# Kernel tuning notes

Hardware: AMD Instinct MI355X
Metric: run time of the kernel (lower is better)

The kernel has to match this reference:

```python
import jax, jax.numpy as jnp
import numpy as np

N_WIRES = 6
N_LAYERS = 4
P = 2
IN_C = 3
OUT_C = 16
B, H, W = 8, 224, 224


def rot_matrix(phi, theta, omega):
    # PennyLane Rot(phi, theta, omega) = RZ(omega) RY(theta) RZ(phi)
    c = jnp.cos(theta * 0.5)
    s = jnp.sin(theta * 0.5)
    ep = jnp.exp(-0.5j * (phi + omega))  # e^{-i(phi+omega)/2}
    em = jnp.exp(-0.5j * (phi - omega))  # e^{-i(phi-omega)/2}
    row0 = jnp.stack([ep * c, -jnp.conj(em) * s])
    row1 = jnp.stack([em * s, jnp.conj(ep) * c])
    return jnp.stack([row0, row1]).astype(jnp.complex64)  # [2,2]


def apply_1q(state, U, wire):
    # state: [N] + [2]*N_WIRES, U: [2,2]
    s = jnp.moveaxis(state, 1 + wire, -1)
    s = jnp.einsum('...i,ji->...j', s, U)
    return jnp.moveaxis(s, -1, 1 + wire)


def apply_cnot(state, c, t):
    s = jnp.moveaxis(state, (1 + c, 1 + t), (-2, -1))
    s = jnp.stack([s[..., 0, :], s[..., 1, ::-1]], axis=-2)
    return jnp.moveaxis(s, (-2, -1), (1 + c, 1 + t))


def _forward(x, weights, fc_w, fc_b, ln_g, ln_b):
    Bx, C, Hx, Wx = x.shape
    p = P
    Hp, Wp = Hx // p, Wx // p
    # unfold + mean over each p x p patch == average pooling
    xm = x.reshape(Bx, C, Hp, p, Wp, p).mean(axis=(3, 5))        # [B,C,Hp,Wp]
    xm = xm.transpose(0, 2, 3, 1).reshape(-1, C)                  # [N,C]
    angles = jnp.pad(xm, ((0, 0), (0, N_WIRES - C)))              # C < n_wires branch
    # AngleEmbedding (RX): product state, RX(a)|0> = [cos(a/2), -i sin(a/2)]
    half = angles * 0.5
    kets = jnp.stack([jnp.cos(half).astype(jnp.complex64),
                      (-1j) * jnp.sin(half).astype(jnp.complex64)], axis=-1)  # [N,6,2]
    state = kets[:, 0]
    for w in range(1, N_WIRES):
        state = jnp.einsum('n...,nj->n...j', state, kets[:, w])  # [N]+[2]*w
    # StronglyEntanglingLayers: Rot on each wire, then CNOT ring with range r
    for l in range(N_LAYERS):
        for w in range(N_WIRES):
            U = rot_matrix(weights[l, w, 0], weights[l, w, 1], weights[l, w, 2])
            state = apply_1q(state, U, w)
        r = (l % (N_WIRES - 1)) + 1
        for w in range(N_WIRES):
            state = apply_cnot(state, w, (w + r) % N_WIRES)
    # <Z_i> expectation values
    probs = state.real ** 2 + state.imag ** 2                     # [N]+[2]*6
    exps = []
    for w in range(N_WIRES):
        axes = tuple(a for a in range(1, N_WIRES + 1) if a != 1 + w)
        pw = probs.sum(axis=axes)                                 # [N,2]
        exps.append(pw[:, 0] - pw[:, 1])
    q = jnp.stack(exps, axis=-1)                                  # [N,6]
    y = q @ fc_w.T + fc_b                                         # [N,16]
    mu = y.mean(-1, keepdims=True)
    var = ((y - mu) ** 2).mean(-1, keepdims=True)
    y = (y - mu) / jnp.sqrt(var + 1e-5) * ln_g + ln_b
    y = jax.nn.relu(y)
    y = y.reshape(Bx, Hp, Wp, OUT_C).transpose(0, 3, 1, 2)        # [B,16,Hp,Wp]
    # F.interpolate(scale=p, bilinear, align_corners=False) == half-pixel bilinear
    return jax.image.resize(y, (Bx, OUT_C, Hx, Wx), method='bilinear')


def setup_inputs() -> dict:
    key = jax.random.key(0)
    ks = jax.random.split(key, 4)
    x = jax.random.normal(ks[0], (B, IN_C, H, W), jnp.float32)
    weights = jax.random.uniform(ks[1], (N_LAYERS, N_WIRES, 3), jnp.float32,
                                 0.0, 2.0 * np.pi)
    fc_w = jax.random.normal(ks[2], (OUT_C, N_WIRES), jnp.float32) * 0.4
    fc_b = jax.random.normal(ks[3], (OUT_C,), jnp.float32) * 0.1
    ln_g = jnp.ones((OUT_C,), jnp.float32)
    ln_b = jnp.zeros((OUT_C,), jnp.float32)
    return {'x': x, 'weights': weights, 'fc_w': fc_w, 'fc_b': fc_b,
            'ln_g': ln_g, 'ln_b': ln_b}


def reference(x, weights, fc_w, fc_b, ln_g, ln_b):
    return _forward(x, weights, fc_w, fc_b, ln_g, ln_b)
```

## Files before the change

### kernel.cpp

```cpp
#include <hip/hip_runtime.h>
#include <math.h>


#define HP 112
#define WP 112

__global__ __launch_bounds__(512) void build_G(const float* __restrict__ wts,
                                               float* __restrict__ S) {
    __shared__ float  U[24][8];
    __shared__ float2 cs[64][9];
    int t = threadIdx.x;
    int lane = t & 63, wv = t >> 6;

    if (t < 24) {
        float phi = wts[t*3+0], th = wts[t*3+1], om = wts[t*3+2];
        float cth, sth, cap, sap, cam, sam;
        sincosf(0.5f*th, &sth, &cth);
        sincosf(0.5f*(phi+om), &sap, &cap);
        sincosf(0.5f*(phi-om), &sam, &cam);
        U[t][0] =  cap*cth; U[t][1] = -sap*cth;
        U[t][2] = -cam*sth; U[t][3] = -sam*sth;
        U[t][4] =  cam*sth; U[t][5] = -sam*sth;
        U[t][6] =  cap*cth; U[t][7] =  sap*cth;
    }
    __syncthreads();

    float2 v = make_float2((lane == (wv << 3)) ? 1.0f : 0.0f, 0.0f);

    for (int l = 0; l < 4; ++l) {
        for (int w = 0; w < 6; ++w) {
            int g = l*6 + w, m = 1 << (5 - w);
            bool hi = (lane & m) != 0;
            float csr = hi ? U[g][6] : U[g][0], csi = hi ? U[g][7] : U[g][1];
            float cpr = hi ? U[g][4] : U[g][2], cpi = hi ? U[g][5] : U[g][3];
            float px = __shfl_xor(v.x, m), py = __shfl_xor(v.y, m);
            v = make_float2(csr*v.x - csi*v.y + cpr*px - cpi*py,
                            csr*v.y + csi*v.x + cpr*py + cpi*px);
        }
        int r = l % 5 + 1;
        for (int w = 0; w < 6; ++w) {
            int mc = 1 << (5 - w), mt = 1 << (5 - ((w + r) % 6));
            float px = __shfl_xor(v.x, mt), py = __shfl_xor(v.y, mt);
            if (lane & mc) v = make_float2(px, py);
        }
    }

    cs[lane][wv] = v;
    __syncthreads();

    if (t < 384) {
        int w = t >> 6, a = (t >> 3) & 7, bb = t & 7;
        if (a <= bb) {
            int mw = 1 << (5 - w);
            float re = 0.f, im = 0.f;
            for (int s = 0; s < 64; ++s) {
                float z = (s & mw) ? -1.f : 1.f;
                float2 va = cs[s][a], vb = cs[s][bb];
                re += z * (va.x*vb.x + va.y*vb.y);
                im += z * (va.x*vb.y - va.y*vb.x);
            }
            int d = (__popc(a) - __popc(bb)) & 3;
            float g = (d == 0) ? re : (d == 1) ? -im : (d == 2) ? -re : im;
            int idx = 8*a - (a*(a-1))/2 + (bb - a);
            S[w*36 + idx] = (a == bb) ? g : 2.0f*g;
        }
    }
}

__global__ __launch_bounds__(256) void fused(
    const float* __restrict__ x, const float* __restrict__ fcw,
    const float* __restrict__ fcb, const float* __restrict__ lng,
    const float* __restrict__ lnb, const float* __restrict__ S,
    float* __restrict__ out) {

    __shared__ __align__(16) float Ss[216];
    __shared__ float fcwS[96], fcbS[16], lngS[16], lnbS[16];
    __shared__ float yS[16][10][18];

    int tid = threadIdx.x;
    int b   = blockIdx.z;
    int ow0 = blockIdx.x * 32, oh0 = blockIdx.y * 16;
    int w0  = blockIdx.x * 16, k0  = blockIdx.y * 8;

    if (tid < 216) Ss[tid] = S[tid];
    for (int i = tid; i < 96;  i += 256) fcwS[i] = fcw[i];
    if (tid < 16) { fcbS[tid] = fcb[tid]; lngS[tid] = lng[tid]; lnbS[tid] = lnb[tid]; }
    __syncthreads();

    if (tid < 180) {
        int pr = tid / 18, pc = tid % 18;
        int ih = min(max(k0 - 1 + pr, 0), HP - 1);
        int iw = min(max(w0 - 1 + pc, 0), WP - 1);

        float m[3];
        #pragma unroll
        for (int c = 0; c < 3; ++c) {
            const float2* px = reinterpret_cast<const float2*>(
                x + (((b*3 + c)*224 + 2*ih)*224 + 2*iw));
            float2 r0 = px[0], r1 = px[112];
            m[c] = 0.25f * (r0.x + r0.y + r1.x + r1.y);
        }

        float cc[3], ssn[3];
        #pragma unroll
        for (int c = 0; c < 3; ++c) __sincosf(0.5f*m[c], &ssn[c], &cc[c]);

        float r8[8] = { cc[0]*cc[1]*cc[2], cc[0]*cc[1]*ssn[2],
                        cc[0]*ssn[1]*cc[2], cc[0]*ssn[1]*ssn[2],
                        ssn[0]*cc[1]*cc[2], ssn[0]*cc[1]*ssn[2],
                        ssn[0]*ssn[1]*cc[2], ssn[0]*ssn[1]*ssn[2] };

        float p[36];
        {
            int k = 0;
            #pragma unroll
            for (int a = 0; a < 8; ++a)
                #pragma unroll
                for (int bb = a; bb < 8; ++bb) p[k++] = r8[a]*r8[bb];
        }

        float q[6];
        #pragma unroll
        for (int w = 0; w < 6; ++w) {
            const float4* S4 = reinterpret_cast<const float4*>(Ss + w*36);
            float acc = 0.f;
            #pragma unroll
            for (int j = 0; j < 9; ++j) {
                float4 s4 = S4[j];
                acc += s4.x*p[j*4+0] + s4.y*p[j*4+1]
                     + s4.z*p[j*4+2] + s4.w*p[j*4+3];
            }
            q[w] = acc;
        }

        float y[16]; float mu = 0.f;
        #pragma unroll
        for (int c = 0; c < 16; ++c) {
            float v = fcbS[c];
            #pragma unroll
            for (int w = 0; w < 6; ++w) v += fcwS[c*6 + w] * q[w];
            y[c] = v; mu += v;
        }
        mu *= 0.0625f;
        float var = 0.f;
        #pragma unroll
        for (int c = 0; c < 16; ++c) { float d = y[c] - mu; var += d*d; }
        var *= 0.0625f;
        float inv = 1.0f / sqrtf(var + 1e-5f);
        #pragma unroll
        for (int c = 0; c < 16; ++c) {
            float vv = (y[c] - mu) * inv * lngS[c] + lnbS[c];
            yS[c][pr][pc] = fmaxf(vv, 0.f);
        }
    }
    __syncthreads();

    #pragma unroll
    for (int k = 0; k < 8; ++k) {
        int it = tid + k * 256;
        int c = it >> 7, rem = it & 127, ohl = rem >> 3, owg = rem & 7;
        int oh = oh0 + ohl, ow = ow0 + owg * 4;
        int kh = oh >> 1, kw = ow >> 1;

        int ha, hb; float wha;
        if (oh & 1) { ha = kh;     hb = min(kh + 1, HP - 1); wha = 0.75f; }
        else        { ha = max(kh - 1, 0); hb = kh;          wha = 0.25f; }
        ha -= (k0 - 1); hb -= (k0 - 1);
        float whb = 1.f - wha;

        int t0 = max(kw - 1, 0)      - (w0 - 1);
        int t1 = kw                  - (w0 - 1);
        int t2 = kw + 1              - (w0 - 1);
        int t3 = min(kw + 2, WP - 1) - (w0 - 1);

        float va0 = wha * yS[c][ha][t0] + whb * yS[c][hb][t0];
        float va1 = wha * yS[c][ha][t1] + whb * yS[c][hb][t1];
        float va2 = wha * yS[c][ha][t2] + whb * yS[c][hb][t2];
        float va3 = wha * yS[c][ha][t3] + whb * yS[c][hb][t3];

        float4 o;
        o.x = 0.25f * va0 + 0.75f * va1;
        o.y = 0.75f * va1 + 0.25f * va2;
        o.z = 0.25f * va1 + 0.75f * va2;
        o.w = 0.75f * va2 + 0.25f * va3;
        *reinterpret_cast<float4*>(out + (((b*16 + c)*224 + oh)*224 + ow)) = o;
    }
}

extern "C" void kernel_launch(void* const* d_in, const int* in_sizes, int n_in,
                              void* d_out, int out_size, void* d_ws, size_t ws_size,
                              hipStream_t stream) {
    const float* x   = (const float*)d_in[0];
    const float* wts = (const float*)d_in[1];
    const float* fcw = (const float*)d_in[2];
    const float* fcb = (const float*)d_in[3];
    const float* lng = (const float*)d_in[4];
    const float* lnb = (const float*)d_in[5];
    float* S   = (float*)d_ws;
    float* out = (float*)d_out;

    build_G<<<1, 512, 0, stream>>>(wts, S);
    fused<<<dim3(7, 14, 8), 256, 0, stream>>>(x, fcw, fcb, lng, lnb, S, out);
}
```

Measured before the change: 84.46 us.

## Fold circuit matrix construction into every block of the fused kernel

Removes the separate single-block build_G launch and has each block of the fused kernel recompute the 6x36 observable matrix itself. Four wavefronts each simulate two basis states of the circuit, and the matrix goes straight into shared memory. The x loads are issued before that work so their latency overlaps it. This saves a kernel launch and the global round trip, but repeats the small circuit simulation in all 784 blocks and adds two barriers before the main work.

```diff
diff --git a/kernel.cpp b/kernel.cpp
--- a/kernel.cpp
+++ b/kernel.cpp
@@ -5,27 +5,59 @@
 #define HP 112
 #define WP 112
 
-__global__ __launch_bounds__(512) void build_G(const float* __restrict__ wts,
-                                               float* __restrict__ S) {
+static __device__ const unsigned char TRI_A[36] = {
+    0,0,0,0,0,0,0,0, 1,1,1,1,1,1,1, 2,2,2,2,2,2, 3,3,3,3,3, 4,4,4,4, 5,5,5, 6,6, 7};
+static __device__ const unsigned char TRI_B[36] = {
+    0,1,2,3,4,5,6,7, 1,2,3,4,5,6,7, 2,3,4,5,6,7, 3,4,5,6,7, 4,5,6,7, 5,6,7, 6,7, 7};
+
+__global__ __launch_bounds__(256) void fused(
+    const float* __restrict__ x, const float* __restrict__ wts,
+    const float* __restrict__ fcw, const float* __restrict__ fcb,
+    const float* __restrict__ lng, const float* __restrict__ lnb,
+    float* __restrict__ out) {
+
     __shared__ float  U[24][8];
     __shared__ float2 cs[64][9];
-    int t = threadIdx.x;
-    int lane = t & 63, wv = t >> 6;
-
-    if (t < 24) {
-        float phi = wts[t*3+0], th = wts[t*3+1], om = wts[t*3+2];
+    __shared__ __align__(16) float Ss[216];
+    __shared__ float fcwS[96], fcbS[16], lngS[16], lnbS[16];
+    __shared__ float yS[16][10][18];
+
+    int tid  = threadIdx.x;
+    int lane = tid & 63, wv = tid >> 6;
+    int b    = blockIdx.z;
+    int ow0  = blockIdx.x * 32, oh0 = blockIdx.y * 16;
+    int w0   = blockIdx.x * 16, k0  = blockIdx.y * 8;
+
+    float2 xr[3][2];
+    int pr = tid / 18, pc = tid % 18;
+    if (tid < 180) {
+        int ih = min(max(k0 - 1 + pr, 0), HP - 1);
+        int iw = min(max(w0 - 1 + pc, 0), WP - 1);
+        #pragma unroll
+        for (int c = 0; c < 3; ++c) {
+            const float2* px = reinterpret_cast<const float2*>(
+                x + (((b*3 + c)*224 + 2*ih)*224 + 2*iw));
+            xr[c][0] = px[0]; xr[c][1] = px[112];
+        }
+    }
+    for (int i = tid; i < 96; i += 256) fcwS[i] = fcw[i];
+    if (tid < 16) { fcbS[tid] = fcb[tid]; lngS[tid] = lng[tid]; lnbS[tid] = lnb[tid]; }
+
+    if (tid < 24) {
+        float phi = wts[tid*3+0], th = wts[tid*3+1], om = wts[tid*3+2];
         float cth, sth, cap, sap, cam, sam;
-        sincosf(0.5f*th, &sth, &cth);
-        sincosf(0.5f*(phi+om), &sap, &cap);
-        sincosf(0.5f*(phi-om), &sam, &cam);
-        U[t][0] =  cap*cth; U[t][1] = -sap*cth;
-        U[t][2] = -cam*sth; U[t][3] = -sam*sth;
-        U[t][4] =  cam*sth; U[t][5] = -sam*sth;
-        U[t][6] =  cap*cth; U[t][7] =  sap*cth;
-    }
-    __syncthreads();
-
-    float2 v = make_float2((lane == (wv << 3)) ? 1.0f : 0.0f, 0.0f);
+        __sincosf(0.5f*th, &sth, &cth);
+        __sincosf(0.5f*(phi+om), &sap, &cap);
+        __sincosf(0.5f*(phi-om), &sam, &cam);
+        U[tid][0] =  cap*cth; U[tid][1] = -sap*cth;
+        U[tid][2] = -cam*sth; U[tid][3] = -sam*sth;
+        U[tid][4] =  cam*sth; U[tid][5] = -sam*sth;
+        U[tid][6] =  cap*cth; U[tid][7] =  sap*cth;
+    }
+    __syncthreads();
+
+    float2 v0 = make_float2((lane == (wv << 3))       ? 1.0f : 0.0f, 0.0f);
+    float2 v1 = make_float2((lane == ((wv + 4) << 3)) ? 1.0f : 0.0f, 0.0f);
 
     for (int l = 0; l < 4; ++l) {
         for (int w = 0; w < 6; ++w) {
@@ -33,77 +65,50 @@
             bool hi = (lane & m) != 0;
             float csr = hi ? U[g][6] : U[g][0], csi = hi ? U[g][7] : U[g][1];
             float cpr = hi ? U[g][4] : U[g][2], cpi = hi ? U[g][5] : U[g][3];
-            float px = __shfl_xor(v.x, m), py = __shfl_xor(v.y, m);
-            v = make_float2(csr*v.x - csi*v.y + cpr*px - cpi*py,
-                            csr*v.y + csi*v.x + cpr*py + cpi*px);
+            float p0x = __shfl_xor(v0.x, m), p0y = __shfl_xor(v0.y, m);
+            float p1x = __shfl_xor(v1.x, m), p1y = __shfl_xor(v1.y, m);
+            v0 = make_float2(csr*v0.x - csi*v0.y + cpr*p0x - cpi*p0y,
+                             csr*v0.y + csi*v0.x + cpr*p0y + cpi*p0x);
+            v1 = make_float2(csr*v1.x - csi*v1.y + cpr*p1x - cpi*p1y,
+                             csr*v1.y + csi*v1.x + cpr*p1y + cpi*p1x);
         }
         int r = l % 5 + 1;
         for (int w = 0; w < 6; ++w) {
             int mc = 1 << (5 - w), mt = 1 << (5 - ((w + r) % 6));
-            float px = __shfl_xor(v.x, mt), py = __shfl_xor(v.y, mt);
-            if (lane & mc) v = make_float2(px, py);
-        }
-    }
-
-    cs[lane][wv] = v;
-    __syncthreads();
-
-    if (t < 384) {
-        int w = t >> 6, a = (t >> 3) & 7, bb = t & 7;
-        if (a <= bb) {
-            int mw = 1 << (5 - w);
-            float re = 0.f, im = 0.f;
-            for (int s = 0; s < 64; ++s) {
-                float z = (s & mw) ? -1.f : 1.f;
-                float2 va = cs[s][a], vb = cs[s][bb];
-                re += z * (va.x*vb.x + va.y*vb.y);
-                im += z * (va.x*vb.y - va.y*vb.x);
-            }
-            int d = (__popc(a) - __popc(bb)) & 3;
-            float g = (d == 0) ? re : (d == 1) ? -im : (d == 2) ? -re : im;
-            int idx = 8*a - (a*(a-1))/2 + (bb - a);
-            S[w*36 + idx] = (a == bb) ? g : 2.0f*g;
-        }
-    }
-}
-
-__global__ __launch_bounds__(256) void fused(
-    const float* __restrict__ x, const float* __restrict__ fcw,
-    const float* __restrict__ fcb, const float* __restrict__ lng,
-    const float* __restrict__ lnb, const float* __restrict__ S,
-    float* __restrict__ out) {
-
-    __shared__ __align__(16) float Ss[216];
-    __shared__ float fcwS[96], fcbS[16], lngS[16], lnbS[16];
-    __shared__ float yS[16][10][18];
-
-    int tid = threadIdx.x;
-    int b   = blockIdx.z;
-    int ow0 = blockIdx.x * 32, oh0 = blockIdx.y * 16;
-    int w0  = blockIdx.x * 16, k0  = blockIdx.y * 8;
-
-    if (tid < 216) Ss[tid] = S[tid];
-    for (int i = tid; i < 96;  i += 256) fcwS[i] = fcw[i];
-    if (tid < 16) { fcbS[tid] = fcb[tid]; lngS[tid] = lng[tid]; lnbS[tid] = lnb[tid]; }
+            float p0x = __shfl_xor(v0.x, mt), p0y = __shfl_xor(v0.y, mt);
+            float p1x = __shfl_xor(v1.x, mt), p1y = __shfl_xor(v1.y, mt);
+            if (lane & mc) { v0 = make_float2(p0x, p0y); v1 = make_float2(p1x, p1y); }
+        }
+    }
+    cs[lane][wv]     = v0;
+    cs[lane][wv + 4] = v1;
+    __syncthreads();
+
+    if (tid < 216) {
+        int w = tid / 36, idx = tid - 36*w;
+        int a = TRI_A[idx], bb = TRI_B[idx];
+        int mw = 1 << (5 - w);
+        float re = 0.f, im = 0.f;
+        #pragma unroll 8
+        for (int s = 0; s < 64; ++s) {
+            float z = (s & mw) ? -1.f : 1.f;
+            float2 va = cs[s][a], vb = cs[s][bb];
+            re += z * (va.x*vb.x + va.y*vb.y);
+            im += z * (va.x*vb.y - va.y*vb.x);
+        }
+        int d = (__popc(a) - __popc(bb)) & 3;
+        float g = (d == 0) ? re : (d == 1) ? -im : (d == 2) ? -re : im;
+        Ss[tid] = (a == bb) ? g : 2.0f*g;
+    }
     __syncthreads();
 
     if (tid < 180) {
-        int pr = tid / 18, pc = tid % 18;
-        int ih = min(max(k0 - 1 + pr, 0), HP - 1);
-        int iw = min(max(w0 - 1 + pc, 0), WP - 1);
-
-        float m[3];
+        float m[3], cc[3], ssn[3];
         #pragma unroll
         for (int c = 0; c < 3; ++c) {
-            const float2* px = reinterpret_cast<const float2*>(
-                x + (((b*3 + c)*224 + 2*ih)*224 + 2*iw));
-            float2 r0 = px[0], r1 = px[112];
-            m[c] = 0.25f * (r0.x + r0.y + r1.x + r1.y);
-        }
-
-        float cc[3], ssn[3];
-        #pragma unroll
-        for (int c = 0; c < 3; ++c) __sincosf(0.5f*m[c], &ssn[c], &cc[c]);
+            m[c] = 0.25f * (xr[c][0].x + xr[c][0].y + xr[c][1].x + xr[c][1].y);
+            __sincosf(0.5f*m[c], &ssn[c], &cc[c]);
+        }
 
         float r8[8] = { cc[0]*cc[1]*cc[2], cc[0]*cc[1]*ssn[2],
                         cc[0]*ssn[1]*cc[2], cc[0]*ssn[1]*ssn[2],
@@ -136,10 +141,10 @@
         float y[16]; float mu = 0.f;
         #pragma unroll
         for (int c = 0; c < 16; ++c) {
-            float v = fcbS[c];
+            float vv = fcbS[c];
             #pragma unroll
-            for (int w = 0; w < 6; ++w) v += fcwS[c*6 + w] * q[w];
-            y[c] = v; mu += v;
+            for (int w = 0; w < 6; ++w) vv += fcwS[c*6 + w] * q[w];
+            y[c] = vv; mu += vv;
         }
         mu *= 0.0625f;
         float var = 0.f;
@@ -163,8 +168,8 @@
         int kh = oh >> 1, kw = ow >> 1;
 
         int ha, hb; float wha;
-        if (oh & 1) { ha = kh;     hb = min(kh + 1, HP - 1); wha = 0.75f; }
-        else        { ha = max(kh - 1, 0); hb = kh;          wha = 0.25f; }
+        if (oh & 1) { ha = kh;             hb = min(kh + 1, HP - 1); wha = 0.75f; }
+        else        { ha = max(kh - 1, 0); hb = kh;                  wha = 0.25f; }
         ha -= (k0 - 1); hb -= (k0 - 1);
         float whb = 1.f - wha;
 
@@ -196,9 +201,7 @@
     const float* fcb = (const float*)d_in[3];
     const float* lng = (const float*)d_in[4];
     const float* lnb = (const float*)d_in[5];
-    float* S   = (float*)d_ws;
     float* out = (float*)d_out;
 
-    build_G<<<1, 512, 0, stream>>>(wts, S);
-    fused<<<dim3(7, 14, 8), 256, 0, stream>>>(x, fcw, fcb, lng, lnb, S, out);
+    fused<<<dim3(7, 14, 8), 256, 0, stream>>>(x, wts, fcw, fcb, lng, lnb, out);
 }
```

New measurement: 95.04 us. 12.5% more time.
